# Optimization experiments

Hardware: AMD Instinct MI355X
Metric: run time of the kernel (lower is better)

The kernel has to match this reference:

```python
import jax, jax.numpy as jnp
import numpy as np

B, S, E, H = 4, 2048, 1024, 16
D = E // H
EPS = 1e-6


def setup_inputs() -> dict:
    key = jax.random.key(0)
    ks = jax.random.split(key, 6)
    glorot = lambda k: jax.random.uniform(k, (E, E), jnp.float32,
                                          -np.sqrt(6.0 / (E + E)), np.sqrt(6.0 / (E + E)))
    return {
        "x": jax.random.normal(ks[0], (B, S, E), jnp.float32),
        "mask": jnp.zeros((B, 1, 1, S), jnp.float32),
        "Wq": glorot(ks[1]), "bq": jnp.zeros((E,), jnp.float32),
        "Wk": glorot(ks[2]), "bk": jnp.zeros((E,), jnp.float32),
        "Wv": glorot(ks[3]), "bv": jnp.zeros((E,), jnp.float32),
        "Wo": glorot(ks[4]), "bo": jnp.zeros((E,), jnp.float32),
        "gamma": jnp.ones((E,), jnp.float32),
        "beta": jnp.zeros((E,), jnp.float32),
    }


def _split_heads(t):
    # [B, S, E] -> [B, H, S, D]
    return t.reshape(B, S, H, D).transpose(0, 2, 1, 3)


def reference(x, mask, Wq, bq, Wk, bk, Wv, bv, Wo, bo, gamma, beta):
    q = _split_heads(x @ Wq + bq)
    k = _split_heads(x @ Wk + bk)
    v = _split_heads(x @ Wv + bv)
    # NOTE: original divides by sqrt(embedding_size), not sqrt(depth)
    scores = jnp.einsum("bhqd,bhkd->bhqk", q, k) / jnp.sqrt(jnp.float32(E))
    scores = scores + mask * (-1e9)
    attn = jax.nn.softmax(scores, axis=-1)
    ctx = jnp.einsum("bhqk,bhkd->bhqd", attn, v)
    ctx = ctx.transpose(0, 2, 1, 3).reshape(B, S, E)
    main_out = ctx @ Wo + bo
    # dropout is identity (is_training=False); residual is the raw input
    added = main_out + x
    mu = jnp.mean(added, axis=-1, keepdims=True)
    var = jnp.mean(jnp.square(added - mu), axis=-1, keepdims=True)
    return gamma * (added - mu) / jnp.sqrt(var + EPS) + beta
```

## Files before the change

kernel.cpp:

```cpp
#include <hip/hip_runtime.h>
#include <hip/hip_bf16.h>


typedef __bf16 bf16_t;
typedef __bf16 bf16x8 __attribute__((ext_vector_type(8)));
typedef __bf16 bf16x4v __attribute__((ext_vector_type(4)));
typedef float f32x4 __attribute__((ext_vector_type(4)));

#define LDS_AS __attribute__((address_space(3)))
#define GLB_AS __attribute__((address_space(1)))

__device__ __forceinline__ void async16(bf16_t* lds, const bf16_t* g) {
  __builtin_amdgcn_global_load_lds((GLB_AS void*)const_cast<bf16_t*>(g),
                                   (LDS_AS void*)lds, 16, 0, 0);
}

__device__ __forceinline__ f32x4 mfma16(bf16x8 a, bf16x8 b, f32x4 c) {
  return __builtin_amdgcn_mfma_f32_16x16x32_bf16(a, b, c, 0, 0, 0);
}

__device__ __forceinline__ float fast_exp2(float x) {
#if __has_builtin(__builtin_amdgcn_exp2f)
  return __builtin_amdgcn_exp2f(x);
#else
  return __expf(x * 0.6931471805599453f);
#endif
}

__global__ __launch_bounds__(256) void cvt_x(const float* __restrict__ x,
                                             bf16_t* __restrict__ xb)
{
  const size_t i = ((size_t)blockIdx.x * 256 + threadIdx.x) * 4;
  const float4 v = *(const float4*)(x + i);
  bf16x4v o;
  o[0] = (bf16_t)v.x; o[1] = (bf16_t)v.y; o[2] = (bf16_t)v.z; o[3] = (bf16_t)v.w;
  *(bf16x4v*)(xb + i) = o;
}

__global__ __launch_bounds__(256) void transpose_k(
    const float* __restrict__ w0, const float* __restrict__ w1,
    const float* __restrict__ w2, const float* __restrict__ w3,
    bf16_t* __restrict__ dst)
{
  __shared__ bf16_t tile[32][33];
  const float* src = (blockIdx.z == 0) ? w0 : (blockIdx.z == 1) ? w1
                   : (blockIdx.z == 2) ? w2 : w3;
  bf16_t* d = dst + (size_t)blockIdx.z * 1024 * 1024;
  const int bx = blockIdx.x * 32, by = blockIdx.y * 32;
  const int tx = threadIdx.x, ty = threadIdx.y;
#pragma unroll
  for (int r = 0; r < 32; r += 8)
    tile[ty + r][tx] = (bf16_t)src[(size_t)(by + ty + r) * 1024 + bx + tx];
  __syncthreads();
#pragma unroll
  for (int r = 0; r < 32; r += 8)
    d[(size_t)(bx + ty + r) * 1024 + by + tx] = tile[tx][ty + r];
}

__global__ __launch_bounds__(256) void gemm_qkv(
    const bf16_t* __restrict__ X, const bf16_t* __restrict__ WtAll,
    const float* __restrict__ bq, const float* __restrict__ bk,
    const float* __restrict__ bv,
    bf16_t* __restrict__ Qb, bf16_t* __restrict__ Kb, bf16_t* __restrict__ Vtb)
{
  __shared__ __align__(16) bf16_t As[128 * 64];
  __shared__ __align__(16) bf16_t Bs[128 * 64];

  const int z = blockIdx.z;
  const bf16_t* Bt = WtAll + (size_t)z * 1024 * 1024;
  const float* bias = (z == 0) ? bq : (z == 1) ? bk : bv;
  const int bm0 = blockIdx.x * 128;
  const int bn0 = blockIdx.y * 128;
  const int t = threadIdx.x;
  const int w = t >> 6, lane = t & 63;
  const int wm = w >> 1, wn = w & 1;
  const int l15 = lane & 15, quad = lane >> 4;
  const int srow8 = lane >> 3;
  const int sp8   = lane & 7;

  f32x4 acc[4][4] = {};

  for (int k0 = 0; k0 < 1024; k0 += 64) {
    __syncthreads();
#pragma unroll
    for (int i = 0; i < 4; ++i) {
      const int row = (w * 4 + i) * 8 + srow8;
      const int c = sp8 ^ (row & 7);
      async16(&As[row * 64 + sp8 * 8], X  + (size_t)(bm0 + row) * 1024 + k0 + c * 8);
      async16(&Bs[row * 64 + sp8 * 8], Bt + (size_t)(bn0 + row) * 1024 + k0 + c * 8);
    }
    __syncthreads();

    bf16x8 af[4][2], bfr[4][2];
#pragma unroll
    for (int mi = 0; mi < 4; ++mi) {
      const int r = wm * 64 + mi * 16 + l15;
#pragma unroll
      for (int kc = 0; kc < 2; ++kc) {
        const int pg = (kc * 4 + quad) ^ (r & 7);
        af[mi][kc] = *(const bf16x8*)&As[r * 64 + pg * 8];
      }
    }
#pragma unroll
    for (int ni = 0; ni < 4; ++ni) {
      const int r = wn * 64 + ni * 16 + l15;
#pragma unroll
      for (int kc = 0; kc < 2; ++kc) {
        const int pg = (kc * 4 + quad) ^ (r & 7);
        bfr[ni][kc] = *(const bf16x8*)&Bs[r * 64 + pg * 8];
      }
    }
#pragma unroll
    for (int kc = 0; kc < 2; ++kc)
#pragma unroll
      for (int mi = 0; mi < 4; ++mi)
#pragma unroll
        for (int ni = 0; ni < 4; ++ni)
          acc[mi][ni] = mfma16(af[mi][kc], bfr[ni][kc], acc[mi][ni]);
  }

  const float QSCALE = 0.045084220f;

#pragma unroll
  for (int ni = 0; ni < 4; ++ni) {
    const int n = bn0 + wn * 64 + ni * 16 + l15;
    const float bb = bias[n];
    const int h = n >> 6, dd = n & 63;
    if (z == 2) {
#pragma unroll
      for (int mi = 0; mi < 4; ++mi) {
        const int m0 = bm0 + wm * 64 + mi * 16 + quad * 4;
        const int bi = m0 >> 11, s = m0 & 2047;
        bf16x4v vk;
#pragma unroll
        for (int r = 0; r < 4; ++r) vk[r] = (bf16_t)(acc[mi][ni][r] + bb);
        *(bf16x4v*)&Vtb[((size_t)(bi * 16 + h) * 64 + dd) * 2048 + s] = vk;
      }
    } else {
#pragma unroll
      for (int mi = 0; mi < 4; ++mi) {
#pragma unroll
        for (int r = 0; r < 4; ++r) {
          const int m = bm0 + wm * 64 + mi * 16 + quad * 4 + r;
          const float v = acc[mi][ni][r] + bb;
          const int bi = m >> 11, s = m & 2047;
          if (z == 0)
            Qb[((size_t)(bi * 16 + h) * 2048 + s) * 64 + dd] = (bf16_t)(v * QSCALE);
          else
            Kb[((size_t)(bi * 16 + h) * 2048 + s) * 64 + dd] = (bf16_t)v;
        }
      }
    }
  }
}

__global__ __launch_bounds__(256) void attn_k(
    const bf16_t* __restrict__ Qb, const bf16_t* __restrict__ Kb,
    const bf16_t* __restrict__ Vtb, const float* __restrict__ mask,
    bf16_t* __restrict__ Ctx)
{
  __shared__ __align__(16) bf16_t Ks[64 * 64];
  __shared__ __align__(16) bf16_t Vs[64 * 64];
  __shared__ __align__(16) bf16_t Ps[128 * 64];
  __shared__ __align__(16) float maskv[64];

  const int qt = blockIdx.x, bh = blockIdx.y;
  const int bi = bh >> 4, h = bh & 15;
  const int q0 = qt * 128;
  const bf16_t* Qh = Qb + (size_t)bh * 2048 * 64;
  const bf16_t* Kh = Kb + (size_t)bh * 2048 * 64;
  const bf16_t* Vh = Vtb + (size_t)bh * 64 * 2048;

  const int t = threadIdx.x;
  const int w = t >> 6, lane = t & 63;
  const int l15 = lane & 15, quad = lane >> 4;

  bf16x8 qb[2][2];
#pragma unroll
  for (int ni = 0; ni < 2; ++ni)
#pragma unroll
    for (int kc = 0; kc < 2; ++kc)
      qb[ni][kc] = *(const bf16x8*)&Qh[(size_t)(q0 + w * 32 + ni * 16 + l15) * 64
                                       + kc * 32 + quad * 8];

  bf16x8 ones;
#pragma unroll
  for (int i = 0; i < 8; ++i) ones[i] = (bf16_t)1.0f;

  f32x4 oacc[4][2] = {};
  f32x4 lacc[2] = {};

  const int srow = lane >> 3;
  const int sp = lane & 7;

  for (int j = 0; j < 32; ++j) {
    const int k0 = j * 64;
    __syncthreads();
#pragma unroll
    for (int i = 0; i < 2; ++i) {
      const int row = (w * 2 + i) * 8 + srow;
      const int c = sp ^ (row & 7);
      async16(&Ks[row * 64 + sp * 8], Kh + (size_t)(k0 + row) * 64 + c * 8);
      async16(&Vs[row * 64 + sp * 8], Vh + (size_t)row * 2048 + k0 + c * 8);
    }
    if (t < 64) maskv[t] = mask[bi * 2048 + k0 + t] * (-1.442695e9f);
    __syncthreads();

    f32x4 sacc[4][2];
#pragma unroll
    for (int mi = 0; mi < 4; ++mi) {
      const float4 mk = *(const float4*)&maskv[mi * 16 + quad * 4];
      f32x4 cinit; cinit[0] = mk.x; cinit[1] = mk.y; cinit[2] = mk.z; cinit[3] = mk.w;
#pragma unroll
      for (int ni = 0; ni < 2; ++ni) sacc[mi][ni] = cinit;
    }
    bf16x8 kf[4][2];
#pragma unroll
    for (int mi = 0; mi < 4; ++mi)
#pragma unroll
      for (int kc = 0; kc < 2; ++kc) {
        const int r = mi * 16 + l15;
        const int pg = (kc * 4 + quad) ^ (r & 7);
        kf[mi][kc] = *(const bf16x8*)&Ks[r * 64 + pg * 8];
      }
#pragma unroll
    for (int mi = 0; mi < 4; ++mi)
#pragma unroll
      for (int ni = 0; ni < 2; ++ni)
#pragma unroll
        for (int kc = 0; kc < 2; ++kc)
          sacc[mi][ni] = mfma16(kf[mi][kc], qb[ni][kc], sacc[mi][ni]);

#pragma unroll
    for (int ni = 0; ni < 2; ++ni) {
      const int row = w * 32 + ni * 16 + l15;
#pragma unroll
      for (int mi = 0; mi < 4; ++mi) {
        bf16x4v pk;
        pk[0] = (bf16_t)fast_exp2(sacc[mi][ni][0]);
        pk[1] = (bf16_t)fast_exp2(sacc[mi][ni][1]);
        pk[2] = (bf16_t)fast_exp2(sacc[mi][ni][2]);
        pk[3] = (bf16_t)fast_exp2(sacc[mi][ni][3]);
        const int pg = (mi * 2 + (quad >> 1)) ^ (row & 7);
        *(bf16x4v*)&Ps[row * 64 + pg * 8 + (quad & 1) * 4] = pk;
      }
    }

    bf16x8 av[4][2], pb[2][2];
#pragma unroll
    for (int ni = 0; ni < 2; ++ni)
#pragma unroll
      for (int kc = 0; kc < 2; ++kc) {
        const int row = w * 32 + ni * 16 + l15;
        const int pg = (kc * 4 + quad) ^ (row & 7);
        pb[ni][kc] = *(const bf16x8*)&Ps[row * 64 + pg * 8];
      }
#pragma unroll
    for (int mi = 0; mi < 4; ++mi)
#pragma unroll
      for (int kc = 0; kc < 2; ++kc) {
        const int r = mi * 16 + l15;
        const int pg = (kc * 4 + quad) ^ (r & 7);
        av[mi][kc] = *(const bf16x8*)&Vs[r * 64 + pg * 8];
      }
#pragma unroll
    for (int mi = 0; mi < 4; ++mi)
#pragma unroll
      for (int ni = 0; ni < 2; ++ni)
#pragma unroll
        for (int kc = 0; kc < 2; ++kc)
          oacc[mi][ni] = mfma16(av[mi][kc], pb[ni][kc], oacc[mi][ni]);
#pragma unroll
    for (int ni = 0; ni < 2; ++ni)
#pragma unroll
      for (int kc = 0; kc < 2; ++kc)
        lacc[ni] = mfma16(ones, pb[ni][kc], lacc[ni]);
  }

#pragma unroll
  for (int ni = 0; ni < 2; ++ni) {
    const float inv = 1.0f / lacc[ni][0];
    const int s = q0 + w * 32 + ni * 16 + l15;
#pragma unroll
    for (int mi = 0; mi < 4; ++mi) {
      bf16x4v o4;
      o4[0] = (bf16_t)(oacc[mi][ni][0] * inv);
      o4[1] = (bf16_t)(oacc[mi][ni][1] * inv);
      o4[2] = (bf16_t)(oacc[mi][ni][2] * inv);
      o4[3] = (bf16_t)(oacc[mi][ni][3] * inv);
      *(bf16x4v*)&Ctx[((size_t)bi * 2048 + s) * 1024 + h * 64 + mi * 16 + quad * 4] = o4;
    }
  }
}

__global__ __launch_bounds__(256) void gemm_proj(
    const bf16_t* __restrict__ Ctx, const bf16_t* __restrict__ WoT,
    const float* __restrict__ bo, const float* __restrict__ Xres,
    float* __restrict__ Add)
{
  __shared__ __align__(16) bf16_t As[128 * 64];
  __shared__ __align__(16) bf16_t Bs[128 * 64];

  const int bm0 = blockIdx.x * 128;
  const int bn0 = blockIdx.y * 128;
  const int t = threadIdx.x;
  const int w = t >> 6, lane = t & 63;
  const int wm = w >> 1, wn = w & 1;
  const int l15 = lane & 15, quad = lane >> 4;
  const int srow8 = lane >> 3;
  const int sp8   = lane & 7;

  f32x4 acc[4][4] = {};

  for (int k0 = 0; k0 < 1024; k0 += 64) {
    __syncthreads();
#pragma unroll
    for (int i = 0; i < 4; ++i) {
      const int row = (w * 4 + i) * 8 + srow8;
      const int c = sp8 ^ (row & 7);
      async16(&As[row * 64 + sp8 * 8], Ctx + (size_t)(bm0 + row) * 1024 + k0 + c * 8);
      async16(&Bs[row * 64 + sp8 * 8], WoT + (size_t)(bn0 + row) * 1024 + k0 + c * 8);
    }
    __syncthreads();

    bf16x8 af[4][2], bfr[4][2];
#pragma unroll
    for (int mi = 0; mi < 4; ++mi) {
      const int r = wm * 64 + mi * 16 + l15;
#pragma unroll
      for (int kc = 0; kc < 2; ++kc) {
        const int pg = (kc * 4 + quad) ^ (r & 7);
        af[mi][kc] = *(const bf16x8*)&As[r * 64 + pg * 8];
      }
    }
#pragma unroll
    for (int ni = 0; ni < 4; ++ni) {
      const int r = wn * 64 + ni * 16 + l15;
#pragma unroll
      for (int kc = 0; kc < 2; ++kc) {
        const int pg = (kc * 4 + quad) ^ (r & 7);
        bfr[ni][kc] = *(const bf16x8*)&Bs[r * 64 + pg * 8];
      }
    }
#pragma unroll
    for (int kc = 0; kc < 2; ++kc)
#pragma unroll
      for (int mi = 0; mi < 4; ++mi)
#pragma unroll
        for (int ni = 0; ni < 4; ++ni)
          acc[mi][ni] = mfma16(af[mi][kc], bfr[ni][kc], acc[mi][ni]);
  }

#pragma unroll
  for (int ni = 0; ni < 4; ++ni) {
    const int n = bn0 + wn * 64 + ni * 16 + l15;
    const float bb = bo[n];
#pragma unroll
    for (int mi = 0; mi < 4; ++mi) {
#pragma unroll
      for (int r = 0; r < 4; ++r) {
        const int m = bm0 + wm * 64 + mi * 16 + quad * 4 + r;
        Add[(size_t)m * 1024 + n] =
            acc[mi][ni][r] + bb + Xres[(size_t)m * 1024 + n];
      }
    }
  }
}

__global__ __launch_bounds__(256) void ln_k(
    const float* __restrict__ A, const float* __restrict__ gamma,
    const float* __restrict__ beta, float* __restrict__ out)
{
  __shared__ float red[8];
  const int row = blockIdx.x, t = threadIdx.x;
  const float4 v = ((const float4*)(A + (size_t)row * 1024))[t];
  float s = v.x + v.y + v.z + v.w;
#pragma unroll
  for (int o = 32; o >= 1; o >>= 1) s += __shfl_xor(s, o);
  if ((t & 63) == 0) red[t >> 6] = s;
  __syncthreads();
  const float mu = (red[0] + red[1] + red[2] + red[3]) * (1.0f / 1024.0f);
  const float dx = v.x - mu, dy = v.y - mu, dz = v.z - mu, dw = v.w - mu;
  float q = dx * dx + dy * dy + dz * dz + dw * dw;
#pragma unroll
  for (int o = 32; o >= 1; o >>= 1) q += __shfl_xor(q, o);
  if ((t & 63) == 0) red[4 + (t >> 6)] = q;
  __syncthreads();
  const float var = (red[4] + red[5] + red[6] + red[7]) * (1.0f / 1024.0f);
  const float rs = rsqrtf(var + 1e-6f);

  const int c0 = t * 4;
  float4 o4;
  o4.x = gamma[c0 + 0] * dx * rs + beta[c0 + 0];
  o4.y = gamma[c0 + 1] * dy * rs + beta[c0 + 1];
  o4.z = gamma[c0 + 2] * dz * rs + beta[c0 + 2];
  o4.w = gamma[c0 + 3] * dw * rs + beta[c0 + 3];
  *(float4*)(out + (size_t)row * 1024 + c0) = o4;
}

extern "C" void kernel_launch(void* const* d_in, const int* in_sizes, int n_in,
                              void* d_out, int out_size, void* d_ws, size_t ws_size,
                              hipStream_t stream)
{
  const float* x     = (const float*)d_in[0];
  const float* mask  = (const float*)d_in[1];
  const float* Wq    = (const float*)d_in[2];
  const float* bq    = (const float*)d_in[3];
  const float* Wk    = (const float*)d_in[4];
  const float* bk    = (const float*)d_in[5];
  const float* Wv    = (const float*)d_in[6];
  const float* bv    = (const float*)d_in[7];
  const float* Wo    = (const float*)d_in[8];
  const float* bo    = (const float*)d_in[9];
  const float* gamma = (const float*)d_in[10];
  const float* beta  = (const float*)d_in[11];
  float* out = (float*)d_out;

  bf16_t* Wt  = (bf16_t*)d_ws;
  bf16_t* Xb  = Wt + (size_t)4 * 1024 * 1024;
  bf16_t* Qb  = Xb + (size_t)8192 * 1024;
  bf16_t* Kb  = Qb + (size_t)8192 * 1024;
  bf16_t* Vtb = Kb + (size_t)8192 * 1024;
  bf16_t* Ctx = Vtb + (size_t)8192 * 1024;
  float*  Add = (float*)(Ctx + (size_t)8192 * 1024);

  cvt_x<<<8192, 256, 0, stream>>>(x, Xb);
  transpose_k<<<dim3(32, 32, 4), dim3(32, 8), 0, stream>>>(Wq, Wk, Wv, Wo, Wt);
  gemm_qkv<<<dim3(64, 8, 3), 256, 0, stream>>>(Xb, Wt, bq, bk, bv, Qb, Kb, Vtb);
  attn_k<<<dim3(16, 64), 256, 0, stream>>>(Qb, Kb, Vtb, mask, Ctx);
  gemm_proj<<<dim3(64, 8), 256, 0, stream>>>(Ctx, Wt + (size_t)3 * 1024 * 1024, bo, x, Add);
  ln_k<<<8192, 256, 0, stream>>>(Add, gamma, beta, out);
}
```

Baseline: 308.0 us.

## Double attention query tile, fuse prep kernels, use one-warp-per-row layernorm

The attention kernel now gives each block 256 query rows, 64 per warp, so every K/V tile loaded into LDS is reused across twice as many queries and the grid halves. The x conversion and weight transposes are merged into one launch to save a kernel launch. LayerNorm processes one row per wavefront using only shuffles, with vectorized gamma/beta loads and no LDS or barriers. The larger attention tile raises register pressure and leaves 512 blocks, which may lower occupancy.

```diff
diff --git a/kernel.cpp b/kernel.cpp
--- a/kernel.cpp
+++ b/kernel.cpp
@@ -27,27 +27,30 @@
 #endif
 }
 
-__global__ __launch_bounds__(256) void cvt_x(const float* __restrict__ x,
-                                             bf16_t* __restrict__ xb)
-{
-  const size_t i = ((size_t)blockIdx.x * 256 + threadIdx.x) * 4;
-  const float4 v = *(const float4*)(x + i);
-  bf16x4v o;
-  o[0] = (bf16_t)v.x; o[1] = (bf16_t)v.y; o[2] = (bf16_t)v.z; o[3] = (bf16_t)v.w;
-  *(bf16x4v*)(xb + i) = o;
-}
-
-__global__ __launch_bounds__(256) void transpose_k(
+__global__ __launch_bounds__(256) void prep_k(
     const float* __restrict__ w0, const float* __restrict__ w1,
     const float* __restrict__ w2, const float* __restrict__ w3,
-    bf16_t* __restrict__ dst)
-{
+    bf16_t* __restrict__ dst,
+    const float* __restrict__ x, bf16_t* __restrict__ xb)
+{
+  const int tx = threadIdx.x, ty = threadIdx.y;
+  if (blockIdx.z == 4) {
+    const int id = (blockIdx.y * 32 + blockIdx.x) * 256 + ty * 32 + tx;
+#pragma unroll
+    for (int it = 0; it < 8; ++it) {
+      const size_t i = ((size_t)id + (size_t)it * 262144) * 4;
+      const float4 v = *(const float4*)(x + i);
+      bf16x4v o;
+      o[0] = (bf16_t)v.x; o[1] = (bf16_t)v.y; o[2] = (bf16_t)v.z; o[3] = (bf16_t)v.w;
+      *(bf16x4v*)(xb + i) = o;
+    }
+    return;
+  }
   __shared__ bf16_t tile[32][33];
   const float* src = (blockIdx.z == 0) ? w0 : (blockIdx.z == 1) ? w1
                    : (blockIdx.z == 2) ? w2 : w3;
   bf16_t* d = dst + (size_t)blockIdx.z * 1024 * 1024;
   const int bx = blockIdx.x * 32, by = blockIdx.y * 32;
-  const int tx = threadIdx.x, ty = threadIdx.y;
 #pragma unroll
   for (int r = 0; r < 32; r += 8)
     tile[ty + r][tx] = (bf16_t)src[(size_t)(by + ty + r) * 1024 + bx + tx];
@@ -161,12 +164,12 @@
 {
   __shared__ __align__(16) bf16_t Ks[64 * 64];
   __shared__ __align__(16) bf16_t Vs[64 * 64];
-  __shared__ __align__(16) bf16_t Ps[128 * 64];
+  __shared__ __align__(16) bf16_t Ps[256 * 64];
   __shared__ __align__(16) float maskv[64];
 
   const int qt = blockIdx.x, bh = blockIdx.y;
   const int bi = bh >> 4, h = bh & 15;
-  const int q0 = qt * 128;
+  const int q0 = qt * 256;
   const bf16_t* Qh = Qb + (size_t)bh * 2048 * 64;
   const bf16_t* Kh = Kb + (size_t)bh * 2048 * 64;
   const bf16_t* Vh = Vtb + (size_t)bh * 64 * 2048;
@@ -175,20 +178,20 @@
   const int w = t >> 6, lane = t & 63;
   const int l15 = lane & 15, quad = lane >> 4;
 
-  bf16x8 qb[2][2];
-#pragma unroll
-  for (int ni = 0; ni < 2; ++ni)
+  bf16x8 qb[4][2];
+#pragma unroll
+  for (int ni = 0; ni < 4; ++ni)
 #pragma unroll
     for (int kc = 0; kc < 2; ++kc)
-      qb[ni][kc] = *(const bf16x8*)&Qh[(size_t)(q0 + w * 32 + ni * 16 + l15) * 64
+      qb[ni][kc] = *(const bf16x8*)&Qh[(size_t)(q0 + w * 64 + ni * 16 + l15) * 64
                                        + kc * 32 + quad * 8];
 
   bf16x8 ones;
 #pragma unroll
   for (int i = 0; i < 8; ++i) ones[i] = (bf16_t)1.0f;
 
-  f32x4 oacc[4][2] = {};
-  f32x4 lacc[2] = {};
+  f32x4 oacc[4][4] = {};
+  f32x4 lacc[4] = {};
 
   const int srow = lane >> 3;
   const int sp = lane & 7;
@@ -206,34 +209,29 @@
     if (t < 64) maskv[t] = mask[bi * 2048 + k0 + t] * (-1.442695e9f);
     __syncthreads();
 
-    f32x4 sacc[4][2];
+    f32x4 sacc[4][4];
 #pragma unroll
     for (int mi = 0; mi < 4; ++mi) {
       const float4 mk = *(const float4*)&maskv[mi * 16 + quad * 4];
       f32x4 cinit; cinit[0] = mk.x; cinit[1] = mk.y; cinit[2] = mk.z; cinit[3] = mk.w;
 #pragma unroll
-      for (int ni = 0; ni < 2; ++ni) sacc[mi][ni] = cinit;
-    }
-    bf16x8 kf[4][2];
-#pragma unroll
-    for (int mi = 0; mi < 4; ++mi)
-#pragma unroll
-      for (int kc = 0; kc < 2; ++kc) {
-        const int r = mi * 16 + l15;
-        const int pg = (kc * 4 + quad) ^ (r & 7);
-        kf[mi][kc] = *(const bf16x8*)&Ks[r * 64 + pg * 8];
-      }
-#pragma unroll
-    for (int mi = 0; mi < 4; ++mi)
-#pragma unroll
-      for (int ni = 0; ni < 2; ++ni)
-#pragma unroll
-        for (int kc = 0; kc < 2; ++kc)
-          sacc[mi][ni] = mfma16(kf[mi][kc], qb[ni][kc], sacc[mi][ni]);
-
-#pragma unroll
-    for (int ni = 0; ni < 2; ++ni) {
-      const int row = w * 32 + ni * 16 + l15;
+      for (int ni = 0; ni < 4; ++ni) sacc[mi][ni] = cinit;
+    }
+#pragma unroll
+    for (int mi = 0; mi < 4; ++mi) {
+      const int r = mi * 16 + l15;
+      const bf16x8 kf0 = *(const bf16x8*)&Ks[r * 64 + ((0 * 4 + quad) ^ (r & 7)) * 8];
+      const bf16x8 kf1 = *(const bf16x8*)&Ks[r * 64 + ((1 * 4 + quad) ^ (r & 7)) * 8];
+#pragma unroll
+      for (int ni = 0; ni < 4; ++ni) {
+        sacc[mi][ni] = mfma16(kf0, qb[ni][0], sacc[mi][ni]);
+        sacc[mi][ni] = mfma16(kf1, qb[ni][1], sacc[mi][ni]);
+      }
+    }
+
+#pragma unroll
+    for (int ni = 0; ni < 4; ++ni) {
+      const int row = w * 64 + ni * 16 + l15;
 #pragma unroll
       for (int mi = 0; mi < 4; ++mi) {
         bf16x4v pk;
@@ -246,41 +244,37 @@
       }
     }
 
-    bf16x8 av[4][2], pb[2][2];
-#pragma unroll
-    for (int ni = 0; ni < 2; ++ni)
+    bf16x8 pb[4][2];
+#pragma unroll
+    for (int ni = 0; ni < 4; ++ni)
 #pragma unroll
       for (int kc = 0; kc < 2; ++kc) {
-        const int row = w * 32 + ni * 16 + l15;
+        const int row = w * 64 + ni * 16 + l15;
         const int pg = (kc * 4 + quad) ^ (row & 7);
         pb[ni][kc] = *(const bf16x8*)&Ps[row * 64 + pg * 8];
       }
 #pragma unroll
-    for (int mi = 0; mi < 4; ++mi)
-#pragma unroll
-      for (int kc = 0; kc < 2; ++kc) {
-        const int r = mi * 16 + l15;
-        const int pg = (kc * 4 + quad) ^ (r & 7);
-        av[mi][kc] = *(const bf16x8*)&Vs[r * 64 + pg * 8];
-      }
-#pragma unroll
-    for (int mi = 0; mi < 4; ++mi)
-#pragma unroll
-      for (int ni = 0; ni < 2; ++ni)
-#pragma unroll
-        for (int kc = 0; kc < 2; ++kc)
-          oacc[mi][ni] = mfma16(av[mi][kc], pb[ni][kc], oacc[mi][ni]);
-#pragma unroll
-    for (int ni = 0; ni < 2; ++ni)
-#pragma unroll
-      for (int kc = 0; kc < 2; ++kc)
-        lacc[ni] = mfma16(ones, pb[ni][kc], lacc[ni]);
-  }
-
-#pragma unroll
-  for (int ni = 0; ni < 2; ++ni) {
+    for (int mi = 0; mi < 4; ++mi) {
+      const int r = mi * 16 + l15;
+      const bf16x8 av0 = *(const bf16x8*)&Vs[r * 64 + ((0 * 4 + quad) ^ (r & 7)) * 8];
+      const bf16x8 av1 = *(const bf16x8*)&Vs[r * 64 + ((1 * 4 + quad) ^ (r & 7)) * 8];
+#pragma unroll
+      for (int ni = 0; ni < 4; ++ni) {
+        oacc[mi][ni] = mfma16(av0, pb[ni][0], oacc[mi][ni]);
+        oacc[mi][ni] = mfma16(av1, pb[ni][1], oacc[mi][ni]);
+      }
+    }
+#pragma unroll
+    for (int ni = 0; ni < 4; ++ni) {
+      lacc[ni] = mfma16(ones, pb[ni][0], lacc[ni]);
+      lacc[ni] = mfma16(ones, pb[ni][1], lacc[ni]);
+    }
+  }
+
+#pragma unroll
+  for (int ni = 0; ni < 4; ++ni) {
     const float inv = 1.0f / lacc[ni][0];
-    const int s = q0 + w * 32 + ni * 16 + l15;
+    const int s = q0 + w * 64 + ni * 16 + l15;
 #pragma unroll
     for (int mi = 0; mi < 4; ++mi) {
       bf16x4v o4;
@@ -371,31 +365,43 @@
     const float* __restrict__ A, const float* __restrict__ gamma,
     const float* __restrict__ beta, float* __restrict__ out)
 {
-  __shared__ float red[8];
-  const int row = blockIdx.x, t = threadIdx.x;
-  const float4 v = ((const float4*)(A + (size_t)row * 1024))[t];
-  float s = v.x + v.y + v.z + v.w;
-#pragma unroll
-  for (int o = 32; o >= 1; o >>= 1) s += __shfl_xor(s, o);
-  if ((t & 63) == 0) red[t >> 6] = s;
-  __syncthreads();
-  const float mu = (red[0] + red[1] + red[2] + red[3]) * (1.0f / 1024.0f);
-  const float dx = v.x - mu, dy = v.y - mu, dz = v.z - mu, dw = v.w - mu;
-  float q = dx * dx + dy * dy + dz * dz + dw * dw;
-#pragma unroll
-  for (int o = 32; o >= 1; o >>= 1) q += __shfl_xor(q, o);
-  if ((t & 63) == 0) red[4 + (t >> 6)] = q;
-  __syncthreads();
-  const float var = (red[4] + red[5] + red[6] + red[7]) * (1.0f / 1024.0f);
-  const float rs = rsqrtf(var + 1e-6f);
-
-  const int c0 = t * 4;
-  float4 o4;
-  o4.x = gamma[c0 + 0] * dx * rs + beta[c0 + 0];
-  o4.y = gamma[c0 + 1] * dy * rs + beta[c0 + 1];
-  o4.z = gamma[c0 + 2] * dz * rs + beta[c0 + 2];
-  o4.w = gamma[c0 + 3] * dw * rs + beta[c0 + 3];
-  *(float4*)(out + (size_t)row * 1024 + c0) = o4;
+  const int wid = threadIdx.x >> 6, lane = threadIdx.x & 63;
+  const int row = blockIdx.x * 4 + wid;
+  const float* a = A + (size_t)row * 1024;
+
+  float4 v[4];
+#pragma unroll
+  for (int k = 0; k < 4; ++k) v[k] = ((const float4*)a)[lane + k * 64];
+
+  float s = 0.f;
+#pragma unroll
+  for (int k = 0; k < 4; ++k) s += (v[k].x + v[k].y) + (v[k].z + v[k].w);
+#pragma unroll
+  for (int o = 1; o < 64; o <<= 1) s += __shfl_xor(s, o);
+  const float mu = s * (1.0f / 1024.0f);
+
+  float q = 0.f;
+#pragma unroll
+  for (int k = 0; k < 4; ++k) {
+    v[k].x -= mu; v[k].y -= mu; v[k].z -= mu; v[k].w -= mu;
+    q += (v[k].x * v[k].x + v[k].y * v[k].y) + (v[k].z * v[k].z + v[k].w * v[k].w);
+  }
+#pragma unroll
+  for (int o = 1; o < 64; o <<= 1) q += __shfl_xor(q, o);
+  const float rs = rsqrtf(q * (1.0f / 1024.0f) + 1e-6f);
+
+#pragma unroll
+  for (int k = 0; k < 4; ++k) {
+    const int c = lane + k * 64;
+    const float4 g4 = ((const float4*)gamma)[c];
+    const float4 b4 = ((const float4*)beta)[c];
+    float4 o4;
+    o4.x = g4.x * v[k].x * rs + b4.x;
+    o4.y = g4.y * v[k].y * rs + b4.y;
+    o4.z = g4.z * v[k].z * rs + b4.z;
+    o4.w = g4.w * v[k].w * rs + b4.w;
+    ((float4*)(out + (size_t)row * 1024))[c] = o4;
+  }
 }
 
 extern "C" void kernel_launch(void* const* d_in, const int* in_sizes, int n_in,
@@ -424,10 +430,9 @@
   bf16_t* Ctx = Vtb + (size_t)8192 * 1024;
   float*  Add = (float*)(Ctx + (size_t)8192 * 1024);
 
-  cvt_x<<<8192, 256, 0, stream>>>(x, Xb);
-  transpose_k<<<dim3(32, 32, 4), dim3(32, 8), 0, stream>>>(Wq, Wk, Wv, Wo, Wt);
+  prep_k<<<dim3(32, 32, 5), dim3(32, 8), 0, stream>>>(Wq, Wk, Wv, Wo, Wt, x, Xb);
   gemm_qkv<<<dim3(64, 8, 3), 256, 0, stream>>>(Xb, Wt, bq, bk, bv, Qb, Kb, Vtb);
-  attn_k<<<dim3(16, 64), 256, 0, stream>>>(Qb, Kb, Vtb, mask, Ctx);
+  attn_k<<<dim3(8, 64), 256, 0, stream>>>(Qb, Kb, Vtb, mask, Ctx);
   gemm_proj<<<dim3(64, 8), 256, 0, stream>>>(Ctx, Wt + (size_t)3 * 1024 * 1024, bo, x, Add);
-  ln_k<<<8192, 256, 0, stream>>>(Add, gamma, beta, out);
-}
+  ln_k<<<2048, 256, 0, stream>>>(Add, gamma, beta, out);
+}
```

After: 300.4 us. -2.5%, faster.
